# Kernel optimization log

Measured on AMD Instinct MI355X. Metric: run time of the kernel, lower is better.

## Reference

```python
import jax, jax.numpy as jnp
import numpy as np

N_NODES = 50000


def gcn_conv(x, W, b, src, dst, ew, n_nodes):
    """PyG GCNConv: out = D^{-1/2}(A + I)D^{-1/2} (x @ W) + b, A weighted by ew.

    Self loops (weight 1) are handled analytically instead of appending edges.
    """
    h = x @ W  # [N, out]
    # degree includes self-loop weight of 1
    deg = jax.ops.segment_sum(ew, dst, num_segments=n_nodes) + 1.0  # [N]
    dinv = jnp.where(deg > 0, jax.lax.rsqrt(deg), 0.0)
    norm = dinv[src] * ew * dinv[dst]  # [E]
    # message = norm * h[src], scatter-add to dst
    agg = jax.ops.segment_sum(h[src] * norm[:, None], dst, num_segments=n_nodes)
    # self-loop contribution: dinv[i] * 1 * dinv[i] * h[i]
    agg = agg + h * (dinv * dinv)[:, None]
    return agg + b


def setup_inputs() -> dict:
    key = jax.random.key(0)
    k = jax.random.split(key, 8)
    n, e, d_in, d_h = N_NODES, 600000, 128, 128
    x = jax.random.normal(k[0], (n, d_in), dtype=jnp.float32)
    edge_index = jax.random.randint(k[1], (2, e), 0, n, dtype=jnp.int64)
    edge_attr = jax.random.uniform(k[2], (e,), dtype=jnp.float32)
    s1 = 1.0 / np.sqrt(d_in)
    s2 = 1.0 / np.sqrt(d_h)
    W1 = jax.random.uniform(k[3], (d_in, d_h), jnp.float32, -s1, s1)
    b1 = jnp.zeros((d_h,), jnp.float32)
    W2 = jax.random.uniform(k[4], (d_h, d_h), jnp.float32, -s2, s2)
    b2 = jnp.zeros((d_h,), jnp.float32)
    return {"x": x, "edge_index": edge_index, "edge_attr": edge_attr,
            "W1": W1, "b1": b1, "W2": W2, "b2": b2}


def reference(x, edge_index, edge_attr, W1, b1, W2, b2):
    src, dst = edge_index[0], edge_index[1]
    h = gcn_conv(x, W1, b1, src, dst, edge_attr, N_NODES)
    h = jax.nn.relu(h)
    # dropout is identity in eval mode (deterministic reference)
    out = gcn_conv(h, W2, b2, src, dst, edge_attr, N_NODES)
    return out
```

## Files before the change

### kernel.cpp

```cpp
#include <hip/hip_runtime.h>
#include <stdint.h>

#define D 128

typedef __bf16 bf16x8 __attribute__((ext_vector_type(8)));
typedef float f32x4 __attribute__((ext_vector_type(4)));

__device__ inline float bf2f(unsigned short u) {
    return __uint_as_float((unsigned)u << 16);
}
__device__ inline unsigned short f2bf(float f) {
    unsigned u = __float_as_uint(f);
    return (unsigned short)((u + 0x7FFF + ((u >> 16) & 1)) >> 16);
}

__global__ __launch_bounds__(256) void k_prep(const float* __restrict__ W1,
                                              unsigned short* __restrict__ Wt1,
                                              const float* __restrict__ W2,
                                              unsigned short* __restrict__ Wt2,
                                              unsigned long long* __restrict__ pk, int n) {
    __shared__ float t[128 * 132];
    const int tid = threadIdx.x;
    if (blockIdx.x < 2) {
        const float* W = (blockIdx.x == 0) ? W1 : W2;
        unsigned short* Wt = (blockIdx.x == 0) ? Wt1 : Wt2;
        for (int i = tid; i < 128 * 32; i += 256) {
            int r = i >> 5, c = i & 31;
            float4 v = *(const float4*)(W + r * 128 + c * 4);
            float* dp = &t[r * 132 + c * 4];
            dp[0] = v.x; dp[1] = v.y; dp[2] = v.z; dp[3] = v.w;
        }
        __syncthreads();
        for (int i = tid; i < 128 * 32; i += 256) {
            int nn = i >> 5, c = i & 31;
            ushort4 o;
            o.x = f2bf(t[(c * 4 + 0) * 132 + nn]);
            o.y = f2bf(t[(c * 4 + 1) * 132 + nn]);
            o.z = f2bf(t[(c * 4 + 2) * 132 + nn]);
            o.w = f2bf(t[(c * 4 + 3) * 132 + nn]);
            *(ushort4*)(Wt + nn * 128 + c * 4) = o;
        }
    } else {
        int i = (blockIdx.x - 2) * 256 + tid;
        if (i < n) pk[i] = 0ULL;
    }
}

template <bool IN_BF16>
__device__ inline void mfma_body(unsigned short* sE,
                                 const void* __restrict__ Xv,
                                 const unsigned short* __restrict__ Wt,
                                 unsigned short* __restrict__ H, int n, int blk) {
    const int tid = threadIdx.x;
    const int row0 = blk * 64;
    const int lane = tid & 63;
    const int wv = tid >> 6;
    const int qm = lane & 15;
    const int quad = lane >> 4;

    const int arow = row0 + wv * 16 + qm;
    const int ar = (arow < n) ? arow : (n - 1);

    f32x4 acc[8];
#pragma unroll
    for (int i = 0; i < 8; ++i) acc[i] = (f32x4){0.f, 0.f, 0.f, 0.f};

#pragma unroll
    for (int kb = 0; kb < 4; ++kb) {
        const int koff = kb * 32 + quad * 8;
        bf16x8 a;
        if (IN_BF16) {
            a = *(const bf16x8*)((const unsigned short*)Xv + (size_t)ar * 128 + koff);
        } else {
            const float* Xf = (const float*)Xv + (size_t)ar * 128 + koff;
            float4 v0 = *(const float4*)(Xf);
            float4 v1 = *(const float4*)(Xf + 4);
            union { bf16x8 v; ushort4 u[2]; } cv;
            cv.u[0].x = f2bf(v0.x); cv.u[0].y = f2bf(v0.y);
            cv.u[0].z = f2bf(v0.z); cv.u[0].w = f2bf(v0.w);
            cv.u[1].x = f2bf(v1.x); cv.u[1].y = f2bf(v1.y);
            cv.u[1].z = f2bf(v1.z); cv.u[1].w = f2bf(v1.w);
            a = cv.v;
        }
#pragma unroll
        for (int n0 = 0; n0 < 8; ++n0) {
            bf16x8 b = *(const bf16x8*)(Wt + (n0 * 16 + qm) * 128 + koff);
            acc[n0] = __builtin_amdgcn_mfma_f32_16x16x32_bf16(a, b, acc[n0], 0, 0, 0);
        }
    }

#pragma unroll
    for (int n0 = 0; n0 < 8; ++n0)
#pragma unroll
        for (int r = 0; r < 4; ++r)
            sE[(wv * 16 + quad * 4 + r) * 136 + n0 * 16 + qm] = f2bf(acc[n0][r]);
    __syncthreads();

    const int row_in = lane >> 2;
    const int c0 = (lane & 3) * 4;
    const int grow = row0 + wv * 16 + row_in;
    if (grow < n) {
#pragma unroll
        for (int j = 0; j < 4; ++j)
            *(int4*)(H + (size_t)grow * 128 + (c0 + j) * 8) =
                *(const int4*)(&sE[(wv * 16 + row_in) * 136 + (c0 + j) * 8]);
    }
}

__global__ __launch_bounds__(256, 4) void k_cm(const float* __restrict__ X,
                                               const unsigned short* __restrict__ Wt,
                                               unsigned short* __restrict__ H, int n, int gb,
                                               const int* __restrict__ ei,
                                               const float* __restrict__ ew,
                                               unsigned long long* __restrict__ pk,
                                               int* __restrict__ rank, int E) {
    __shared__ unsigned short sE[64 * 136];
    if (blockIdx.x < gb) {
        mfma_body<false>(sE, (const void*)X, Wt, H, n, blockIdx.x);
    } else {
        const int base = (blockIdx.x - gb) * 1024 + threadIdx.x;
        int d[4]; float w[4];
        bool ok[4];
#pragma unroll
        for (int k = 0; k < 4; ++k) {
            int e = base + k * 256;
            ok[k] = (e < E);
            d[k] = ok[k] ? ei[E + e] : 0;
            w[k] = ok[k] ? ew[e] : 0.f;
        }
#pragma unroll
        for (int k = 0; k < 4; ++k) {
            if (ok[k]) {
                unsigned int fx = (unsigned int)(w[k] * 16777216.0f);
                unsigned long long old =
                    atomicAdd(&pk[d[k]], (1ULL << 32) | (unsigned long long)fx);
                rank[base + k * 256] = (int)(old >> 32);
            }
        }
    }
}

__global__ __launch_bounds__(256, 4) void k_mfma2(const unsigned short* __restrict__ X,
                                                  const unsigned short* __restrict__ Wt,
                                                  unsigned short* __restrict__ H, int n) {
    __shared__ unsigned short sE[64 * 136];
    mfma_body<true>(sE, (const void*)X, Wt, H, n, blockIdx.x);
}

__global__ __launch_bounds__(256) void k_scanA(const unsigned long long* __restrict__ pk,
                                               int* rowstart, int* bsums, int n) {
    __shared__ int tmp[256];
    int tid = threadIdx.x;
    int i = blockIdx.x * 256 + tid;
    int v = (i < n) ? (int)(pk[i] >> 32) : 0;
    tmp[tid] = v;
    __syncthreads();
    for (int off = 1; off < 256; off <<= 1) {
        int t = (tid >= off) ? tmp[tid - off] : 0;
        __syncthreads();
        tmp[tid] += t;
        __syncthreads();
    }
    if (i < n) rowstart[i] = tmp[tid] - v;
    if (tid == 255) bsums[blockIdx.x] = tmp[255];
}

__global__ __launch_bounds__(256) void k_scanBC(int* rowstart, const int* __restrict__ bsums,
                                                const unsigned long long* __restrict__ pk,
                                                int* cnt, float* dinv, int n) {
    __shared__ int sred[4];
    int tid = threadIdx.x;
    int v = (tid < (int)blockIdx.x) ? bsums[tid] : 0;
#pragma unroll
    for (int off = 32; off; off >>= 1) v += __shfl_down(v, off);
    if ((tid & 63) == 0) sred[tid >> 6] = v;
    __syncthreads();
    int total = sred[0] + sred[1] + sred[2] + sred[3];
    int i = blockIdx.x * 256 + tid;
    if (i < n) {
        rowstart[i] += total;
        unsigned long long pv = pk[i];
        cnt[i] = (int)(pv >> 32);
        float deg = 1.0f + (float)(unsigned int)(pv & 0xFFFFFFFFu) * (1.0f / 16777216.0f);
        dinv[i] = rsqrtf(deg);
    }
}

__global__ __launch_bounds__(256) void k_edges(const int* __restrict__ ei,
                                               const float* __restrict__ ew,
                                               const float* __restrict__ dinv,
                                               const int* __restrict__ rowstart,
                                               const int* __restrict__ rank,
                                               int2* __restrict__ erec, int E) {
    const int base = blockIdx.x * 512 + threadIdx.x;
#pragma unroll
    for (int k = 0; k < 2; ++k) {
        int e = base + k * 256;
        if (e < E) {
            int s = ei[e];
            int d = ei[E + e];
            int p = rowstart[d] + rank[e];
            float nm = dinv[s] * ew[e] * dinv[d];
            erec[p] = make_int2(s, __float_as_int(nm));
        }
    }
}

template <bool OUT_BF16>
__global__ __launch_bounds__(256) void k_gather(const ushort4* __restrict__ H4,
                                                const int2* __restrict__ erec,
                                                const int* __restrict__ rowstart,
                                                const int* __restrict__ cnt,
                                                const float* __restrict__ dinv,
                                                const float4* __restrict__ bias4,
                                                void* __restrict__ OUTv, int n) {
    const int lane = threadIdx.x & 31;
    const int node = blockIdx.x * 8 + (threadIdx.x >> 5);
    if (node >= n) return;
    const int start = rowstart[node];
    const int m = cnt[node];
    const float di = dinv[node];
    const float dii = di * di;

    float4 b = bias4[lane];
    ushort4 h = H4[(size_t)node * 32 + lane];
    float ax = b.x + dii * bf2f(h.x);
    float ay = b.y + dii * bf2f(h.y);
    float az = b.z + dii * bf2f(h.z);
    float aw = b.w + dii * bf2f(h.w);

    int j = 0;
    for (; j + 4 <= m; j += 4) {
        const int base = start + j;
        int2 e0 = erec[base + 0], e1 = erec[base + 1];
        int2 e2 = erec[base + 2], e3 = erec[base + 3];
        float w0 = __int_as_float(e0.y), w1 = __int_as_float(e1.y);
        float w2 = __int_as_float(e2.y), w3 = __int_as_float(e3.y);
        ushort4 v0 = H4[(size_t)e0.x * 32 + lane];
        ushort4 v1 = H4[(size_t)e1.x * 32 + lane];
        ushort4 v2 = H4[(size_t)e2.x * 32 + lane];
        ushort4 v3 = H4[(size_t)e3.x * 32 + lane];
        ax += w0 * bf2f(v0.x); ay += w0 * bf2f(v0.y); az += w0 * bf2f(v0.z); aw += w0 * bf2f(v0.w);
        ax += w1 * bf2f(v1.x); ay += w1 * bf2f(v1.y); az += w1 * bf2f(v1.z); aw += w1 * bf2f(v1.w);
        ax += w2 * bf2f(v2.x); ay += w2 * bf2f(v2.y); az += w2 * bf2f(v2.z); aw += w2 * bf2f(v2.w);
        ax += w3 * bf2f(v3.x); ay += w3 * bf2f(v3.y); az += w3 * bf2f(v3.z); aw += w3 * bf2f(v3.w);
    }
    for (; j < m; ++j) {
        int2 er = erec[start + j];
        float w = __int_as_float(er.y);
        ushort4 v = H4[(size_t)er.x * 32 + lane];
        ax += w * bf2f(v.x); ay += w * bf2f(v.y); az += w * bf2f(v.z); aw += w * bf2f(v.w);
    }
    if (OUT_BF16) {
        ushort4 o;
        o.x = f2bf(fmaxf(ax, 0.f)); o.y = f2bf(fmaxf(ay, 0.f));
        o.z = f2bf(fmaxf(az, 0.f)); o.w = f2bf(fmaxf(aw, 0.f));
        ((ushort4*)OUTv)[(size_t)node * 32 + lane] = o;
    } else {
        float4 o; o.x = ax; o.y = ay; o.z = az; o.w = aw;
        ((float4*)OUTv)[(size_t)node * 32 + lane] = o;
    }
}

extern "C" void kernel_launch(void* const* d_in, const int* in_sizes, int n_in,
                              void* d_out, int out_size, void* d_ws, size_t ws_size,
                              hipStream_t stream) {
    const float* x  = (const float*)d_in[0];
    const int*   ei = (const int*)d_in[1];
    const float* ew = (const float*)d_in[2];
    const float* W1 = (const float*)d_in[3];
    const float* b1 = (const float*)d_in[4];
    const float* W2 = (const float*)d_in[5];
    const float* b2 = (const float*)d_in[6];
    float* out = (float*)d_out;

    const int N = in_sizes[0] / D;
    const int E = in_sizes[2];

    char* p = (char*)d_ws;
    auto alloc = [&](size_t bytes) {
        void* r = (void*)p;
        p += (bytes + 255) & ~(size_t)255;
        return r;
    };
    unsigned long long* pk = (unsigned long long*)alloc((size_t)N * 8);
    float* dinv     = (float*)alloc((size_t)N * 4);
    int*   cnt      = (int*)alloc((size_t)N * 4);
    int*   rowstart = (int*)alloc((size_t)N * 4);
    int*   bsums    = (int*)alloc(1024 * 4);
    int*   rank     = (int*)alloc((size_t)E * 4);
    int2*  erec     = (int2*)alloc((size_t)E * 8);
    unsigned short* B1  = (unsigned short*)alloc((size_t)N * D * 2);
    unsigned short* B2h = (unsigned short*)alloc((size_t)N * D * 2);
    unsigned short* Wt1 = (unsigned short*)alloc(128 * 128 * 2);
    unsigned short* Wt2 = (unsigned short*)alloc(128 * 128 * 2);

    const int nb  = (N + 255) / 256;
    const int eb2 = (E + 511) / 512;
    const int eb4 = (E + 1023) / 1024;
    const int gb  = (N + 63) / 64;
    const int hb  = (N + 7) / 8;

    k_prep<<<2 + nb, 256, 0, stream>>>(W1, Wt1, W2, Wt2, pk, N);
    k_cm<<<gb + eb4, 256, 0, stream>>>(x, Wt1, B1, N, gb, ei, ew, pk, rank, E);
    k_scanA<<<nb, 256, 0, stream>>>(pk, rowstart, bsums, N);
    k_scanBC<<<nb, 256, 0, stream>>>(rowstart, bsums, pk, cnt, dinv, N);
    k_edges<<<eb2, 256, 0, stream>>>(ei, ew, dinv, rowstart, rank, erec, E);
    k_gather<true><<<hb, 256, 0, stream>>>((const ushort4*)B1, erec, rowstart, cnt,
                                           dinv, (const float4*)b1, (void*)B2h, N);
    k_mfma2<<<gb, 256, 0, stream>>>(B2h, Wt2, B1, N);
    k_gather<false><<<hb, 256, 0, stream>>>((const ushort4*)B1, erec, rowstart, cnt,
                                            dinv, (const float4*)b2, (void*)out, N);
}
```

Baseline: 231.1 us.

## Replace global-atomic CSR build with two-level bucketed counting sort

Rewrites CSR construction from per-edge 64-bit global atomics on node counters into a two-level radix sort. Edges are first bucketed into 128-node chunks using per-block LDS histograms plus a scan, then each chunk is sorted locally in LDS, where degrees and norms are also computed. This is meant to remove heavy global atomic contention and scattered rank writes. It adds more kernels and an extra pass over the edge records. Packing dst and src into 16 bits each assumes node ids below 65536, and the row order is now nondeterministic, so float sum order changes.

```diff
diff --git a/kernel.cpp b/kernel.cpp
--- a/kernel.cpp
+++ b/kernel.cpp
@@ -2,6 +2,8 @@
 #include <stdint.h>
 
 #define D 128
+#define EPB 4096
+#define CSZ 128
 
 typedef __bf16 bf16x8 __attribute__((ext_vector_type(8)));
 typedef float f32x4 __attribute__((ext_vector_type(4)));
@@ -17,32 +19,26 @@
 __global__ __launch_bounds__(256) void k_prep(const float* __restrict__ W1,
                                               unsigned short* __restrict__ Wt1,
                                               const float* __restrict__ W2,
-                                              unsigned short* __restrict__ Wt2,
-                                              unsigned long long* __restrict__ pk, int n) {
+                                              unsigned short* __restrict__ Wt2) {
     __shared__ float t[128 * 132];
     const int tid = threadIdx.x;
-    if (blockIdx.x < 2) {
-        const float* W = (blockIdx.x == 0) ? W1 : W2;
-        unsigned short* Wt = (blockIdx.x == 0) ? Wt1 : Wt2;
-        for (int i = tid; i < 128 * 32; i += 256) {
-            int r = i >> 5, c = i & 31;
-            float4 v = *(const float4*)(W + r * 128 + c * 4);
-            float* dp = &t[r * 132 + c * 4];
-            dp[0] = v.x; dp[1] = v.y; dp[2] = v.z; dp[3] = v.w;
-        }
-        __syncthreads();
-        for (int i = tid; i < 128 * 32; i += 256) {
-            int nn = i >> 5, c = i & 31;
-            ushort4 o;
-            o.x = f2bf(t[(c * 4 + 0) * 132 + nn]);
-            o.y = f2bf(t[(c * 4 + 1) * 132 + nn]);
-            o.z = f2bf(t[(c * 4 + 2) * 132 + nn]);
-            o.w = f2bf(t[(c * 4 + 3) * 132 + nn]);
-            *(ushort4*)(Wt + nn * 128 + c * 4) = o;
-        }
-    } else {
-        int i = (blockIdx.x - 2) * 256 + tid;
-        if (i < n) pk[i] = 0ULL;
+    const float* W = (blockIdx.x == 0) ? W1 : W2;
+    unsigned short* Wt = (blockIdx.x == 0) ? Wt1 : Wt2;
+    for (int i = tid; i < 128 * 32; i += 256) {
+        int r = i >> 5, c = i & 31;
+        float4 v = *(const float4*)(W + r * 128 + c * 4);
+        float* dp = &t[r * 132 + c * 4];
+        dp[0] = v.x; dp[1] = v.y; dp[2] = v.z; dp[3] = v.w;
+    }
+    __syncthreads();
+    for (int i = tid; i < 128 * 32; i += 256) {
+        int nn = i >> 5, c = i & 31;
+        ushort4 o;
+        o.x = f2bf(t[(c * 4 + 0) * 132 + nn]);
+        o.y = f2bf(t[(c * 4 + 1) * 132 + nn]);
+        o.z = f2bf(t[(c * 4 + 2) * 132 + nn]);
+        o.w = f2bf(t[(c * 4 + 3) * 132 + nn]);
+        *(ushort4*)(Wt + nn * 128 + c * 4) = o;
     }
 }
 
@@ -107,35 +103,155 @@
     }
 }
 
-__global__ __launch_bounds__(256, 4) void k_cm(const float* __restrict__ X,
-                                               const unsigned short* __restrict__ Wt,
-                                               unsigned short* __restrict__ H, int n, int gb,
-                                               const int* __restrict__ ei,
-                                               const float* __restrict__ ew,
-                                               unsigned long long* __restrict__ pk,
-                                               int* __restrict__ rank, int E) {
-    __shared__ unsigned short sE[64 * 136];
+__global__ __launch_bounds__(256, 4) void k_histmfma(const float* __restrict__ X,
+                                                     const unsigned short* __restrict__ Wt,
+                                                     unsigned short* __restrict__ H, int n, int gb,
+                                                     const int* __restrict__ ei,
+                                                     unsigned int* __restrict__ bh,
+                                                     int E, int C) {
+    __shared__ char arena[64 * 136 * 2];
     if (blockIdx.x < gb) {
-        mfma_body<false>(sE, (const void*)X, Wt, H, n, blockIdx.x);
+        mfma_body<false>((unsigned short*)arena, (const void*)X, Wt, H, n, blockIdx.x);
     } else {
-        const int base = (blockIdx.x - gb) * 1024 + threadIdx.x;
-        int d[4]; float w[4];
-        bool ok[4];
-#pragma unroll
-        for (int k = 0; k < 4; ++k) {
+        unsigned int* hist = (unsigned int*)arena;
+        const int b = blockIdx.x - gb;
+        for (int i = threadIdx.x; i < C; i += 256) hist[i] = 0;
+        __syncthreads();
+        const int base = b * EPB + threadIdx.x;
+#pragma unroll
+        for (int k = 0; k < EPB / 256; ++k) {
             int e = base + k * 256;
-            ok[k] = (e < E);
-            d[k] = ok[k] ? ei[E + e] : 0;
-            w[k] = ok[k] ? ew[e] : 0.f;
-        }
-#pragma unroll
-        for (int k = 0; k < 4; ++k) {
-            if (ok[k]) {
-                unsigned int fx = (unsigned int)(w[k] * 16777216.0f);
-                unsigned long long old =
-                    atomicAdd(&pk[d[k]], (1ULL << 32) | (unsigned long long)fx);
-                rank[base + k * 256] = (int)(old >> 32);
-            }
+            if (e < E) atomicAdd(&hist[((unsigned)ei[E + e]) >> 7], 1u);
+        }
+        __syncthreads();
+        for (int i = threadIdx.x; i < C; i += 256)
+            bh[(size_t)b * C + i] = hist[i];
+    }
+}
+
+__global__ __launch_bounds__(256) void k_scanA2(const unsigned int* __restrict__ bh,
+                                                int* __restrict__ ebase, int* __restrict__ bsums,
+                                                int total, int C, int B1) {
+    __shared__ int tmp[256];
+    const int tid = threadIdx.x;
+    const int i = blockIdx.x * 256 + tid;
+    int v = 0;
+    if (i < total) {
+        int c = i / B1;
+        int b = i - c * B1;
+        v = (int)bh[(size_t)b * C + c];
+    }
+    tmp[tid] = v;
+    __syncthreads();
+    for (int off = 1; off < 256; off <<= 1) {
+        int t = (tid >= off) ? tmp[tid - off] : 0;
+        __syncthreads();
+        tmp[tid] += t;
+        __syncthreads();
+    }
+    if (i < total) ebase[i] = tmp[tid] - v;
+    if (tid == 255) bsums[blockIdx.x] = tmp[255];
+}
+
+__global__ __launch_bounds__(256) void k_scanB2(int* __restrict__ ebase,
+                                                const int* __restrict__ bsums, int total) {
+    __shared__ int sred[4];
+    const int tid = threadIdx.x;
+    int v = (tid < (int)blockIdx.x) ? bsums[tid] : 0;
+#pragma unroll
+    for (int off = 32; off; off >>= 1) v += __shfl_down(v, off);
+    if ((tid & 63) == 0) sred[tid >> 6] = v;
+    __syncthreads();
+    int tot = sred[0] + sred[1] + sred[2] + sred[3];
+    int i = blockIdx.x * 256 + tid;
+    if (i < total) ebase[i] += tot;
+}
+
+__global__ __launch_bounds__(256) void k_scat(const int* __restrict__ ei,
+                                              const float* __restrict__ ew,
+                                              const int* __restrict__ ebase,
+                                              int2* __restrict__ brec, int E, int C, int B1) {
+    __shared__ unsigned int cur[512];
+    const int b = blockIdx.x;
+    for (int i = threadIdx.x; i < C; i += 256) cur[i] = 0;
+    __syncthreads();
+    const int base = b * EPB + threadIdx.x;
+#pragma unroll
+    for (int k = 0; k < EPB / 256; ++k) {
+        int e = base + k * 256;
+        if (e < E) {
+            int s = ei[e];
+            unsigned d = (unsigned)ei[E + e];
+            float w = ew[e];
+            int c = d >> 7;
+            unsigned r = atomicAdd(&cur[c], 1u);
+            int pos = ebase[c * B1 + b] + (int)r;
+            brec[pos] = make_int2((int)((d << 16) | (unsigned)s), __float_as_int(w));
+        }
+    }
+}
+
+__global__ __launch_bounds__(256) void k_cbuild(const int2* __restrict__ brec,
+                                                const int* __restrict__ ebase,
+                                                int2* __restrict__ erec,
+                                                int* __restrict__ rowstart,
+                                                int* __restrict__ cnt,
+                                                float* __restrict__ dinv,
+                                                int n, int C, int B1, int E) {
+    __shared__ unsigned int hcnt[CSZ], hdeg[CSZ], lsc[CSZ], curs[CSZ];
+    const int c = blockIdx.x;
+    const int tid = threadIdx.x;
+    const int cs = ebase[c * B1];
+    const int ce = (c + 1 < C) ? ebase[(c + 1) * B1] : E;
+    if (tid < CSZ) { hcnt[tid] = 0; hdeg[tid] = 0; }
+    __syncthreads();
+    for (int i = cs + tid; i < ce; i += 256) {
+        int2 r = brec[i];
+        int local = (int)(((unsigned)r.x) >> 16) & (CSZ - 1);
+        atomicAdd(&hcnt[local], 1u);
+        atomicAdd(&hdeg[local], (unsigned)(__int_as_float(r.y) * 16777216.0f));
+    }
+    __syncthreads();
+    if (tid < CSZ) lsc[tid] = hcnt[tid];
+    __syncthreads();
+    for (int off = 1; off < CSZ; off <<= 1) {
+        unsigned t = (tid < CSZ && tid >= off) ? lsc[tid - off] : 0u;
+        __syncthreads();
+        if (tid < CSZ) lsc[tid] += t;
+        __syncthreads();
+    }
+    if (tid < CSZ) {
+        unsigned excl = lsc[tid] - hcnt[tid];
+        curs[tid] = excl;
+        int node = c * CSZ + tid;
+        if (node < n) {
+            rowstart[node] = cs + (int)excl;
+            cnt[node] = (int)hcnt[tid];
+            float deg = 1.0f + (float)hdeg[tid] * (1.0f / 16777216.0f);
+            dinv[node] = rsqrtf(deg);
+        }
+    }
+    __syncthreads();
+    for (int i = cs + tid; i < ce; i += 256) {
+        int2 r = brec[i];
+        int local = (int)(((unsigned)r.x) >> 16) & (CSZ - 1);
+        unsigned rk = atomicAdd(&curs[local], 1u);
+        erec[cs + (int)rk] = r;
+    }
+}
+
+__global__ __launch_bounds__(256) void k_nrm(int2* __restrict__ erec,
+                                             const float* __restrict__ dinv, int E) {
+    const int base = blockIdx.x * 512 + threadIdx.x;
+#pragma unroll
+    for (int k = 0; k < 2; ++k) {
+        int e = base + k * 256;
+        if (e < E) {
+            int2 r = erec[e];
+            unsigned dst = ((unsigned)r.x) >> 16;
+            int src = r.x & 0xFFFF;
+            float nm = dinv[src] * __int_as_float(r.y) * dinv[dst];
+            erec[e] = make_int2(src, __float_as_int(nm));
         }
     }
 }
@@ -145,65 +261,6 @@
                                                   unsigned short* __restrict__ H, int n) {
     __shared__ unsigned short sE[64 * 136];
     mfma_body<true>(sE, (const void*)X, Wt, H, n, blockIdx.x);
-}
-
-__global__ __launch_bounds__(256) void k_scanA(const unsigned long long* __restrict__ pk,
-                                               int* rowstart, int* bsums, int n) {
-    __shared__ int tmp[256];
-    int tid = threadIdx.x;
-    int i = blockIdx.x * 256 + tid;
-    int v = (i < n) ? (int)(pk[i] >> 32) : 0;
-    tmp[tid] = v;
-    __syncthreads();
-    for (int off = 1; off < 256; off <<= 1) {
-        int t = (tid >= off) ? tmp[tid - off] : 0;
-        __syncthreads();
-        tmp[tid] += t;
-        __syncthreads();
-    }
-    if (i < n) rowstart[i] = tmp[tid] - v;
-    if (tid == 255) bsums[blockIdx.x] = tmp[255];
-}
-
-__global__ __launch_bounds__(256) void k_scanBC(int* rowstart, const int* __restrict__ bsums,
-                                                const unsigned long long* __restrict__ pk,
-                                                int* cnt, float* dinv, int n) {
-    __shared__ int sred[4];
-    int tid = threadIdx.x;
-    int v = (tid < (int)blockIdx.x) ? bsums[tid] : 0;
-#pragma unroll
-    for (int off = 32; off; off >>= 1) v += __shfl_down(v, off);
-    if ((tid & 63) == 0) sred[tid >> 6] = v;
-    __syncthreads();
-    int total = sred[0] + sred[1] + sred[2] + sred[3];
-    int i = blockIdx.x * 256 + tid;
-    if (i < n) {
-        rowstart[i] += total;
-        unsigned long long pv = pk[i];
-        cnt[i] = (int)(pv >> 32);
-        float deg = 1.0f + (float)(unsigned int)(pv & 0xFFFFFFFFu) * (1.0f / 16777216.0f);
-        dinv[i] = rsqrtf(deg);
-    }
-}
-
-__global__ __launch_bounds__(256) void k_edges(const int* __restrict__ ei,
-                                               const float* __restrict__ ew,
-                                               const float* __restrict__ dinv,
-                                               const int* __restrict__ rowstart,
-                                               const int* __restrict__ rank,
-                                               int2* __restrict__ erec, int E) {
-    const int base = blockIdx.x * 512 + threadIdx.x;
-#pragma unroll
-    for (int k = 0; k < 2; ++k) {
-        int e = base + k * 256;
-        if (e < E) {
-            int s = ei[e];
-            int d = ei[E + e];
-            int p = rowstart[d] + rank[e];
-            float nm = dinv[s] * ew[e] * dinv[d];
-            erec[p] = make_int2(s, __float_as_int(nm));
-        }
-    }
 }
 
 template <bool OUT_BF16>
@@ -277,38 +334,43 @@
     const int N = in_sizes[0] / D;
     const int E = in_sizes[2];
 
+    const int C  = (N + CSZ - 1) / CSZ;
+    const int B1n = (E + EPB - 1) / EPB;
+    const int total = C * B1n;
+    const int sb = (total + 255) / 256;
+
     char* p = (char*)d_ws;
     auto alloc = [&](size_t bytes) {
         void* r = (void*)p;
         p += (bytes + 255) & ~(size_t)255;
         return r;
     };
-    unsigned long long* pk = (unsigned long long*)alloc((size_t)N * 8);
+    unsigned int* bh = (unsigned int*)alloc((size_t)total * 4);
+    int*   ebase    = (int*)alloc((size_t)total * 4);
+    int*   bsums    = (int*)alloc(1024 * 4);
     float* dinv     = (float*)alloc((size_t)N * 4);
     int*   cnt      = (int*)alloc((size_t)N * 4);
     int*   rowstart = (int*)alloc((size_t)N * 4);
-    int*   bsums    = (int*)alloc(1024 * 4);
-    int*   rank     = (int*)alloc((size_t)E * 4);
+    int2*  brec     = (int2*)alloc((size_t)E * 8);
     int2*  erec     = (int2*)alloc((size_t)E * 8);
-    unsigned short* B1  = (unsigned short*)alloc((size_t)N * D * 2);
-    unsigned short* B2h = (unsigned short*)alloc((size_t)N * D * 2);
-    unsigned short* Wt1 = (unsigned short*)alloc(128 * 128 * 2);
-    unsigned short* Wt2 = (unsigned short*)alloc(128 * 128 * 2);
-
-    const int nb  = (N + 255) / 256;
-    const int eb2 = (E + 511) / 512;
-    const int eb4 = (E + 1023) / 1024;
-    const int gb  = (N + 63) / 64;
-    const int hb  = (N + 7) / 8;
-
-    k_prep<<<2 + nb, 256, 0, stream>>>(W1, Wt1, W2, Wt2, pk, N);
-    k_cm<<<gb + eb4, 256, 0, stream>>>(x, Wt1, B1, N, gb, ei, ew, pk, rank, E);
-    k_scanA<<<nb, 256, 0, stream>>>(pk, rowstart, bsums, N);
-    k_scanBC<<<nb, 256, 0, stream>>>(rowstart, bsums, pk, cnt, dinv, N);
-    k_edges<<<eb2, 256, 0, stream>>>(ei, ew, dinv, rowstart, rank, erec, E);
-    k_gather<true><<<hb, 256, 0, stream>>>((const ushort4*)B1, erec, rowstart, cnt,
-                                           dinv, (const float4*)b1, (void*)B2h, N);
-    k_mfma2<<<gb, 256, 0, stream>>>(B2h, Wt2, B1, N);
-    k_gather<false><<<hb, 256, 0, stream>>>((const ushort4*)B1, erec, rowstart, cnt,
+    unsigned short* Hbuf = (unsigned short*)alloc((size_t)N * D * 2);
+    unsigned short* Abuf = (unsigned short*)alloc((size_t)N * D * 2);
+    unsigned short* Wt1  = (unsigned short*)alloc(128 * 128 * 2);
+    unsigned short* Wt2  = (unsigned short*)alloc(128 * 128 * 2);
+
+    const int gb = (N + 63) / 64;
+    const int hb = (N + 7) / 8;
+
+    k_prep<<<2, 256, 0, stream>>>(W1, Wt1, W2, Wt2);
+    k_histmfma<<<gb + B1n, 256, 0, stream>>>(x, Wt1, Hbuf, N, gb, ei, bh, E, C);
+    k_scanA2<<<sb, 256, 0, stream>>>(bh, ebase, bsums, total, C, B1n);
+    k_scanB2<<<sb, 256, 0, stream>>>(ebase, bsums, total);
+    k_scat<<<B1n, 256, 0, stream>>>(ei, ew, ebase, brec, E, C, B1n);
+    k_cbuild<<<C, 256, 0, stream>>>(brec, ebase, erec, rowstart, cnt, dinv, N, C, B1n, E);
+    k_nrm<<<(E + 511) / 512, 256, 0, stream>>>(erec, dinv, E);
+    k_gather<true><<<hb, 256, 0, stream>>>((const ushort4*)Hbuf, erec, rowstart, cnt,
+                                           dinv, (const float4*)b1, (void*)Abuf, N);
+    k_mfma2<<<gb, 256, 0, stream>>>(Abuf, Wt2, Hbuf, N);
+    k_gather<false><<<hb, 256, 0, stream>>>((const ushort4*)Hbuf, erec, rowstart, cnt,
                                             dinv, (const float4*)b2, (void*)out, N);
 }
```

After: 220.9 us. 1.05x faster.
